# Kernel optimization log

Measured on AMD Instinct MI355X. Metric: run time of the kernel, lower is better.

Reference implementation:

```python
import jax, jax.numpy as jnp
import numpy as np

E = 32  # embedding_dim
B = 1048576

def setup_inputs() -> dict:
    key = jax.random.key(0)
    ks = jax.random.split(key, 16)
    def p(k, shape, scale=0.1):
        return jax.random.normal(k, shape, dtype=jnp.float32) * scale
    return {
        'x': jax.random.normal(ks[0], (B, 2, 5), dtype=jnp.float32),
        'fc_emb_w': p(ks[1], (E, 5)), 'fc_emb_b': p(ks[2], (E,)),
        'in_proj_w': p(ks[3], (3 * E, E)), 'in_proj_b': p(ks[4], (3 * E,)),
        'out_proj_w': p(ks[5], (E, E)), 'out_proj_b': p(ks[6], (E,)),
        'w_ih': p(ks[7], (E, E)), 'b_ih': p(ks[8], (E,)),
        'w_hh': p(ks[9], (E, E)), 'b_hh': p(ks[10], (E,)),
        'fc_dec_w': p(ks[11], (5, E)), 'fc_dec_b': p(ks[12], (5,)),
        'out_w': p(ks[13], (3, 5)), 'out_b': p(ks[14], (3,)),
    }

def gelu(x):
    return jax.nn.gelu(x, approximate=False)  # torch nn.GELU default (erf)

def reference(x, fc_emb_w, fc_emb_b, in_proj_w, in_proj_b,
              out_proj_w, out_proj_b, w_ih, b_ih, w_hh, b_hh,
              fc_dec_w, fc_dec_b, out_w, out_b):
    # per-token embedding: [B,2,5] -> [B,2,E]
    e = gelu(jnp.einsum('bsi,ei->bse', x, fc_emb_w) + fc_emb_b)
    # single-head self-attention (seq_len=2)
    wq, wk, wv = jnp.split(in_proj_w, 3, axis=0)
    bq, bk, bv = jnp.split(in_proj_b, 3, axis=0)
    q = jnp.einsum('bsd,ed->bse', e, wq) + bq
    k = jnp.einsum('bsd,ed->bse', e, wk) + bk
    v = jnp.einsum('bsd,ed->bse', e, wv) + bv
    scores = jnp.einsum('bqd,bkd->bqk', q, k) / jnp.sqrt(jnp.float32(E))
    attn = jax.nn.softmax(scores, axis=-1)
    o = jnp.einsum('bqk,bkd->bqd', attn, v)
    o = jnp.einsum('bsd,ed->bse', o, out_proj_w) + out_proj_b
    # 2-step tanh RNN, h0 = 0; final hidden state only
    h1 = jnp.tanh(o[:, 0] @ w_ih.T + b_ih + b_hh)
    h2 = jnp.tanh(o[:, 1] @ w_ih.T + b_ih + h1 @ w_hh.T + b_hh)
    # decode
    d = gelu(h2 @ fc_dec_w.T + fc_dec_b)
    return d @ out_w.T + out_b  # [B,3]
```

## Files before the change

kernel.cpp:

```cpp
#include <hip/hip_runtime.h>
#include <math.h>

#define BT 256

typedef _Float16 half2v __attribute__((ext_vector_type(2)));
typedef __fp16   fp16x2 __attribute__((ext_vector_type(2)));
typedef _Float16 half8  __attribute__((ext_vector_type(8)));
typedef float    f32x16 __attribute__((ext_vector_type(16)));

union U4H8 { unsigned int u[4]; half8 h; };

__device__ __forceinline__ half2v u2h(unsigned int u){
  union { unsigned int u; half2v h; } c; c.u = u; return c.h;
}
__device__ __forceinline__ unsigned int h2u(half2v h){
  union { unsigned int u; half2v h; } c; c.h = h; return c.u;
}
__device__ __forceinline__ half2v pkrtz(float a, float b){
  union { fp16x2 f; half2v h; } c;
  c.f = __builtin_amdgcn_cvt_pkrtz(a, b);
  return c.h;
}
__device__ __forceinline__ float fdot2(half2v a, half2v b, float c){
  return __builtin_amdgcn_fdot2(a, b, c, false);
}
__device__ __forceinline__ float frcp(float x){ return __builtin_amdgcn_rcpf(x); }

__device__ __forceinline__ unsigned int pk_rne(float a, float b){
  half2v h; h.x = (_Float16)a; h.y = (_Float16)b; return h2u(h);
}

__device__ __forceinline__ half2v gelu_pk(half2v x){
  const _Float16 a0 = (_Float16)0.3989423f,  a1 = (_Float16)-0.0663157f,
                 a2 = (_Float16)0.0096298f,  a3 = (_Float16)-0.00095967f,
                 a4 = (_Float16)0.000048f,   hp = (_Float16)0.5f,
                 hn = (_Float16)-0.5f;
  const half2v A0={a0,a0}, A1={a1,a1}, A2={a2,a2}, A3={a3,a3}, A4={a4,a4};
  const half2v HP={hp,hp}, HN={hn,hn};
  half2v t = x*x;
  half2v q = A4*t + A3;
  q = q*t + A2;
  q = q*t + A1;
  q = q*t + A0;
  half2v u = x*q;
#if __has_builtin(__builtin_elementwise_min)
  u = __builtin_elementwise_max(u, HN);
  u = __builtin_elementwise_min(u, HP);
#else
  u.x = u.x > hp ? hp : (u.x < hn ? hn : u.x);
  u.y = u.y > hp ? hp : (u.y < hn ? hn : u.y);
#endif
  return x*(u + HP);
}

__device__ __forceinline__ half2v tanh_pk(half2v x){
  const _Float16 c0=(_Float16)0.999716f,  c1=(_Float16)-0.328107f,
                 c2=(_Float16)0.116352f,  c3=(_Float16)-0.031255f,
                 c4=(_Float16)0.005038f,  c5=(_Float16)-0.000348f,
                 tp=(_Float16)2.0f,       tn=(_Float16)-2.0f;
  const half2v C0={c0,c0},C1={c1,c1},C2={c2,c2},C3={c3,c3},C4={c4,c4},C5={c5,c5};
  const half2v TP={tp,tp}, TN={tn,tn};
#if __has_builtin(__builtin_elementwise_min)
  x = __builtin_elementwise_max(x, TN);
  x = __builtin_elementwise_min(x, TP);
#else
  x.x = x.x > tp ? tp : (x.x < tn ? tn : x.x);
  x.y = x.y > tp ? tp : (x.y < tn ? tn : x.y);
#endif
  half2v t = x*x;
  half2v p = C5*t + C4;
  p = p*t + C3;
  p = p*t + C2;
  p = p*t + C1;
  p = p*t + C0;
  return x*p;
}

__global__ void prep_kernel(const float* __restrict__ inw, const float* __restrict__ inb,
                            const float* __restrict__ opw, const float* __restrict__ opb,
                            const float* __restrict__ wih, const float* __restrict__ bih,
                            const float* __restrict__ bhh, const float* __restrict__ whh,
                            const float* __restrict__ decw, const float* __restrict__ embw,
                            const float* __restrict__ embb,
                            const float* __restrict__ decb, const float* __restrict__ outw,
                            unsigned int* __restrict__ wsu){
  __shared__ float sQ[1024], sK[1024], sV[1024], sOP[1024], sWI[1024];
  __shared__ float sA[1024], sP[1024], sM[1024], sT[32], sWV[32];
  const float ISS = 0.17677669529663689f;
  int t = threadIdx.x;
  sQ[t]  = inw[t];
  sK[t]  = inw[1024 + t];
  sV[t]  = inw[2048 + t];
  sOP[t] = opw[t];
  sWI[t] = wih[t];
  __syncthreads();
  int tx = t & 31, ty = t >> 5;
  float accA = 0.f, accP = 0.f;
  #pragma unroll
  for (int m = 0; m < 32; m++){
    accA += sQ[m*32 + ty] * sK[m*32 + tx];
    accP += sOP[ty*32 + m] * sV[m*32 + tx];
  }
  sA[ty*32 + tx] = accA;
  sP[ty*32 + tx] = accP;
  if (ty == 0){
    float aw = 0.f;
    #pragma unroll
    for (int m = 0; m < 32; m++) aw += inb[m] * sK[m*32 + tx];
    sWV[tx] = aw;
  }
  if (ty == 1){
    float at = opb[tx];
    #pragma unroll
    for (int m = 0; m < 32; m++) at += sOP[tx*32 + m] * inb[64 + m];
    sT[tx] = at;
  }
  __syncthreads();
  float accM = 0.f;
  #pragma unroll
  for (int m = 0; m < 32; m++) accM += sWI[ty*32 + m] * sP[m*32 + tx];
  sM[ty*32 + tx] = accM;
  if (ty == 2){
    float ab = bih[tx] + bhh[tx];
    #pragma unroll
    for (int m = 0; m < 32; m++) ab += sWI[tx*32 + m] * sT[m];
    ((float*)wsu)[2320 + tx] = ab;
  }
  __syncthreads();
  if (t < 512){
    int r = t >> 4, j = t & 15;
    int c0 = 16*(j>>3) + 8*((j>>1)&1) + 4*((j>>2)&1) + 2*(j&1);
    wsu[t]        = pk_rne(ISS*sA[r*32+c0], ISS*sA[r*32+c0+1]);
    wsu[512 + t]  = pk_rne(sM[r*32+c0],  sM[r*32+c0+1]);
    wsu[1024 + t] = pk_rne(whh[r*32+c0], whh[r*32+c0+1]);
    wsu[1536 + t] = (r < 5) ? pk_rne(decw[r*32+c0], decw[r*32+c0+1]) : 0u;
  } else if (t < 768){
    int q = t - 512, j2 = q >> 3, cc = (q & 7)*2;
    float a = (cc   < 5) ? embw[j2*5+cc]   : 0.f;
    float b = (cc+1 < 5) ? embw[j2*5+cc+1] : ((cc+1 == 5) ? embb[j2] : 0.f);
    wsu[2048 + q] = pk_rne(a, b);
  } else if (t < 784){
    int q = t - 768, gg = q >> 3, j = q & 7;
    int r0 = 2*(j&1) + 8*(j>>1) + 4*gg;
    wsu[2304 + q] = pk_rne(ISS*sWV[r0], ISS*sWV[r0+1]);
  } else if (t < 787){
    int i = t - 784, c = 2*i;
    float a = decb[c];
    float b = (c+1 < 5) ? decb[c+1] : 0.f;
    wsu[2352 + i] = pk_rne(a, b);
  } else if (t < 796){
    int q = t - 787;
    int r = (q >= 6) ? 2 : ((q >= 3) ? 1 : 0);
    int p = q - r*3, c = 2*p;
    float a = outw[r*5 + c];
    float b = (c+1 < 5) ? outw[r*5 + c + 1] : 0.f;
    wsu[2355 + q] = pk_rne(a, b);
  }
}

__device__ __forceinline__ half8 ldfrag(const unsigned int* __restrict__ p){
  U4H8 t; t.u[0]=p[0]; t.u[1]=p[1]; t.u[2]=p[2]; t.u[3]=p[3]; return t.h;
}
__device__ __forceinline__ half8 h8of(const unsigned int* q){
  U4H8 t; t.u[0]=q[0]; t.u[1]=q[1]; t.u[2]=q[2]; t.u[3]=q[3]; return t.h;
}

__device__ __forceinline__ f32x16 ldbias(const float* __restrict__ p, int grp){
  const float4* b = (const float4*)(p + 4*grp);
  float4 q0 = b[0], q1 = b[2], q2 = b[4], q3 = b[6];
  f32x16 c;
  c[0]=q0.x; c[1]=q0.y; c[2]=q0.z; c[3]=q0.w;
  c[4]=q1.x; c[5]=q1.y; c[6]=q1.z; c[7]=q1.w;
  c[8]=q2.x; c[9]=q2.y; c[10]=q2.z; c[11]=q2.w;
  c[12]=q3.x; c[13]=q3.y; c[14]=q3.z; c[15]=q3.w;
  return c;
}

__global__ __launch_bounds__(BT, 4) void fused_kernel(
    const float* __restrict__ x,
    const unsigned int* __restrict__ wsu,
    const float* __restrict__ outb,
    float* __restrict__ y, long long B)
{
  int tid  = threadIdx.x;
  int lane = tid & 63;
  int col  = lane & 31;
  bool g   = (lane >> 5) != 0;
  int grp  = g ? 1 : 0;
  long long eBase = ((long long)blockIdx.x*(BT/64) + (tid>>6)) * 64;
  if (eBase >= B) return;

  const unsigned int* pA = wsu;
  const unsigned int* pM = wsu + 512;
  const unsigned int* pW = wsu + 1024;
  const unsigned int* pD = wsu + 1536;
  const unsigned int* pE = wsu + 2048;
  const unsigned int* pwv = wsu + 2304;
  const float* bMf = (const float*)(wsu + 2320);
  const unsigned int* pdb  = wsu + 2352;
  const unsigned int* pout = wsu + 2355;

  half8 embA = ldfrag(pE + col*8  + grp*4);
  half8 A1   = ldfrag(pA + col*16 + grp*4), A2 = ldfrag(pA + col*16 + 8 + grp*4);
  half8 M1   = ldfrag(pM + col*16 + grp*4), M2 = ldfrag(pM + col*16 + 8 + grp*4);
  half8 W1   = ldfrag(pW + col*16 + grp*4), W2 = ldfrag(pW + col*16 + 8 + grp*4);
  half8 D1   = ldfrag(pD + col*16 + grp*4), D2 = ldfrag(pD + col*16 + 8 + grp*4);
  half2v wv[8];
  #pragma unroll
  for (int j = 0; j < 8; j++) wv[j] = u2h(pwv[grp*8 + j]);

  f32x16 cb_bM = ldbias(bMf, grp);
  f32x16 z16;
  #pragma unroll
  for (int i = 0; i < 16; i++) z16[i] = 0.f;

  U4H8 xb0[2], xb1[2];
  #pragma unroll
  for (int tt = 0; tt < 2; tt++){
    long long e = eBase + 32*tt + col;
    if (e >= B) e = B - 1;
    const float2* xp = (const float2*)(x + e*10ll);
    float2 p0 = xp[0], p1 = xp[1], p2 = xp[2], p3 = xp[3], p4 = xp[4];
    xb0[tt].u[0] = g ? 0u : h2u(pkrtz(p0.x, p0.y));
    xb0[tt].u[1] = g ? 0u : h2u(pkrtz(p1.x, p1.y));
    xb0[tt].u[2] = g ? 0u : h2u(pkrtz(p2.x, 1.0f));
    xb0[tt].u[3] = 0u;
    xb1[tt].u[0] = g ? 0u : h2u(pkrtz(p2.y, p3.x));
    xb1[tt].u[1] = g ? 0u : h2u(pkrtz(p3.y, p4.x));
    xb1[tt].u[2] = g ? 0u : h2u(pkrtz(p4.y, 1.0f));
    xb1[tt].u[3] = 0u;
  }

  f32x16 e0D[2], e1D[2];
  #pragma unroll
  for (int tt = 0; tt < 2; tt++){
    e0D[tt] = __builtin_amdgcn_mfma_f32_32x32x16_f16(embA, xb0[tt].h, z16, 0,0,0);
    e1D[tt] = __builtin_amdgcn_mfma_f32_32x32x16_f16(embA, xb1[tt].h, z16, 0,0,0);
  }
  unsigned int epk[2][8], dlpk[2][8];
  #pragma unroll
  for (int tt = 0; tt < 2; tt++){
    #pragma unroll
    for (int i = 0; i < 8; i++){
      half2v e0h = gelu_pk(pkrtz(e0D[tt][2*i], e0D[tt][2*i+1]));
      half2v e1h = gelu_pk(pkrtz(e1D[tt][2*i], e1D[tt][2*i+1]));
      epk[tt][i]  = h2u(e0h);
      dlpk[tt][i] = h2u(e1h - e0h);
    }
  }

  f32x16 gD[2];
  #pragma unroll
  for (int tt = 0; tt < 2; tt++){
    gD[tt] = __builtin_amdgcn_mfma_f32_32x32x16_f16(A1, h8of(dlpk[tt]), z16, 0,0,0);
    gD[tt] = __builtin_amdgcn_mfma_f32_32x32x16_f16(A2, h8of(dlpk[tt]+4), gD[tt], 0,0,0);
  }
  float a01[2], a11[2];
  #pragma unroll
  for (int tt = 0; tt < 2; tt++){
    float t0 = 0.f, t1 = 0.f, dw = 0.f;
    #pragma unroll
    for (int i = 0; i < 8; i++){
      half2v gp = pkrtz(gD[tt][2*i], gD[tt][2*i+1]);
      t0 = fdot2(u2h(epk[tt][i]),  gp, t0);
      t1 = fdot2(u2h(dlpk[tt][i]), gp, t1);
      dw = fdot2(wv[i], u2h(dlpk[tt][i]), dw);
    }
    t0 += __shfl_xor(t0, 32);
    t1 += __shfl_xor(t1, 32);
    dw += __shfl_xor(dw, 32);
    a01[tt] = frcp(1.0f + __expf(-(t0      + dw)));
    a11[tt] = frcp(1.0f + __expf(-(t0 + t1 + dw)));
  }

  unsigned int c0pk[2][8], c1pk[2][8];
  #pragma unroll
  for (int tt = 0; tt < 2; tt++){
    _Float16 q01 = (_Float16)a01[tt], qda = (_Float16)(a11[tt] - a01[tt]);
    half2v s01 = {q01,q01}, sda = {qda,qda};
    #pragma unroll
    for (int j = 0; j < 8; j++){
      half2v c0 = u2h(dlpk[tt][j])*s01 + u2h(epk[tt][j]);
      half2v c1 = u2h(dlpk[tt][j])*sda + c0;
      c0pk[tt][j] = h2u(c0); c1pk[tt][j] = h2u(c1);
    }
  }

  f32x16 h1D[2];
  #pragma unroll
  for (int tt = 0; tt < 2; tt++){
    h1D[tt] = __builtin_amdgcn_mfma_f32_32x32x16_f16(M1, h8of(c0pk[tt]), cb_bM, 0,0,0);
    h1D[tt] = __builtin_amdgcn_mfma_f32_32x32x16_f16(M2, h8of(c0pk[tt]+4), h1D[tt], 0,0,0);
  }
  unsigned int h1pk[2][8];
  #pragma unroll
  for (int tt = 0; tt < 2; tt++)
    #pragma unroll
    for (int i = 0; i < 8; i++)
      h1pk[tt][i] = h2u(tanh_pk(pkrtz(h1D[tt][2*i], h1D[tt][2*i+1])));

  f32x16 h2D[2];
  #pragma unroll
  for (int tt = 0; tt < 2; tt++){
    h2D[tt] = __builtin_amdgcn_mfma_f32_32x32x16_f16(M1, h8of(c1pk[tt]), cb_bM, 0,0,0);
    h2D[tt] = __builtin_amdgcn_mfma_f32_32x32x16_f16(M2, h8of(c1pk[tt]+4), h2D[tt], 0,0,0);
    h2D[tt] = __builtin_amdgcn_mfma_f32_32x32x16_f16(W1, h8of(h1pk[tt]),   h2D[tt], 0,0,0);
    h2D[tt] = __builtin_amdgcn_mfma_f32_32x32x16_f16(W2, h8of(h1pk[tt]+4), h2D[tt], 0,0,0);
  }
  unsigned int h2pk[2][8];
  #pragma unroll
  for (int tt = 0; tt < 2; tt++)
    #pragma unroll
    for (int i = 0; i < 8; i++)
      h2pk[tt][i] = h2u(tanh_pk(pkrtz(h2D[tt][2*i], h2D[tt][2*i+1])));

  f32x16 dvD[2];
  #pragma unroll
  for (int tt = 0; tt < 2; tt++){
    dvD[tt] = __builtin_amdgcn_mfma_f32_32x32x16_f16(D1, h8of(h2pk[tt]), z16, 0,0,0);
    dvD[tt] = __builtin_amdgcn_mfma_f32_32x32x16_f16(D2, h8of(h2pk[tt]+4), dvD[tt], 0,0,0);
  }
  #pragma unroll
  for (int tt = 0; tt < 2; tt++){
    float dv4 = __shfl_xor(dvD[tt][0], 32);
    half2v dp0 = pkrtz(dvD[tt][0], dvD[tt][1]) + u2h(pdb[0]);
    half2v dp1 = pkrtz(dvD[tt][2], dvD[tt][3]) + u2h(pdb[1]);
    half2v dp2 = pkrtz(dv4,        0.f       ) + u2h(pdb[2]);
    dp0 = gelu_pk(dp0); dp1 = gelu_pk(dp1); dp2 = gelu_pk(dp2);
    float y0 = fdot2(u2h(pout[0]), dp0, fdot2(u2h(pout[1]), dp1, fdot2(u2h(pout[2]), dp2, outb[0])));
    float y1 = fdot2(u2h(pout[3]), dp0, fdot2(u2h(pout[4]), dp1, fdot2(u2h(pout[5]), dp2, outb[1])));
    float y2 = fdot2(u2h(pout[6]), dp0, fdot2(u2h(pout[7]), dp1, fdot2(u2h(pout[8]), dp2, outb[2])));
    long long e = eBase + 32*tt + col;
    if (lane < 32 && e < B){
      float* yp = y + e*3ll;
      yp[0] = y0; yp[1] = y1; yp[2] = y2;
    }
  }
}

extern "C" void kernel_launch(void* const* d_in, const int* in_sizes, int n_in,
                              void* d_out, int out_size, void* d_ws, size_t ws_size,
                              hipStream_t stream){
  const float* x    = (const float*)d_in[0];
  const float* embw = (const float*)d_in[1];
  const float* embb = (const float*)d_in[2];
  const float* inw  = (const float*)d_in[3];
  const float* inb  = (const float*)d_in[4];
  const float* opw  = (const float*)d_in[5];
  const float* opb  = (const float*)d_in[6];
  const float* wih  = (const float*)d_in[7];
  const float* bih  = (const float*)d_in[8];
  const float* whh  = (const float*)d_in[9];
  const float* bhh  = (const float*)d_in[10];
  const float* decw = (const float*)d_in[11];
  const float* decb = (const float*)d_in[12];
  const float* outw = (const float*)d_in[13];
  const float* outb = (const float*)d_in[14];
  float* y = (float*)d_out;
  unsigned int* wsu = (unsigned int*)d_ws;

  long long B = in_sizes[0] / 10;
  long long elems_per_block = (BT/64) * 64;

  prep_kernel<<<1, 1024, 0, stream>>>(inw, inb, opw, opb, wih, bih, bhh,
                                      whh, decw, embw, embb, decb, outw, wsu);
  int grid = (int)((B + elems_per_block - 1)/elems_per_block);
  fused_kernel<<<grid, BT, 0, stream>>>(x, wsu, outb, y, B);
}
```

Baseline: 136.2 us.

## Loop each block over two tiles and swap cross-half shuffles for permlane32_swap

Each block now processes two consecutive 256-element tiles in a loop and the grid is halved. This amortizes the per-wave loading of weight fragments, biases and output bias across more elements. Cross-half reductions use permlane32_swap when the builtin is available instead of ds_bpermute-based shuffles, and the input loads are skipped entirely for the upper half-wave. The price is fewer waves in flight, which could cut latency hiding on the load-bound path.

```diff
diff --git a/kernel.cpp b/kernel.cpp
--- a/kernel.cpp
+++ b/kernel.cpp
@@ -2,6 +2,7 @@
 #include <math.h>
 
 #define BT 256
+#define ITERS 2
 
 typedef _Float16 half2v __attribute__((ext_vector_type(2)));
 typedef __fp16   fp16x2 __attribute__((ext_vector_type(2)));
@@ -28,6 +29,31 @@
 
 __device__ __forceinline__ unsigned int pk_rne(float a, float b){
   half2v h; h.x = (_Float16)a; h.y = (_Float16)b; return h2u(h);
+}
+
+#if __has_builtin(__builtin_amdgcn_permlane32_swap)
+#define HAVE_PLSWAP 1
+#endif
+
+__device__ __forceinline__ float red_sum32(float v){
+#ifdef HAVE_PLSWAP
+  union { float f; unsigned u; } c; c.f = v;
+  auto r = __builtin_amdgcn_permlane32_swap(c.u, c.u, false, false);
+  union { unsigned u; float f; } a, b; a.u = r[0]; b.u = r[1];
+  return a.f + b.f;
+#else
+  return v + __shfl_xor(v, 32);
+#endif
+}
+__device__ __forceinline__ float upper_to_lower(float v){
+#ifdef HAVE_PLSWAP
+  union { float f; unsigned u; } c; c.f = v;
+  auto r = __builtin_amdgcn_permlane32_swap(c.u, c.u, false, false);
+  union { unsigned u; float f; } b; b.u = r[1];
+  return b.f;
+#else
+  return __shfl_xor(v, 32);
+#endif
 }
 
 __device__ __forceinline__ half2v gelu_pk(half2v x){
@@ -187,8 +213,6 @@
   int col  = lane & 31;
   bool g   = (lane >> 5) != 0;
   int grp  = g ? 1 : 0;
-  long long eBase = ((long long)blockIdx.x*(BT/64) + (tid>>6)) * 64;
-  if (eBase >= B) return;
 
   const unsigned int* pA = wsu;
   const unsigned int* pM = wsu + 512;
@@ -210,130 +234,141 @@
   for (int j = 0; j < 8; j++) wv[j] = u2h(pwv[grp*8 + j]);
 
   f32x16 cb_bM = ldbias(bMf, grp);
+  float ob0 = outb[0], ob1 = outb[1], ob2 = outb[2];
   f32x16 z16;
   #pragma unroll
   for (int i = 0; i < 16; i++) z16[i] = 0.f;
 
-  U4H8 xb0[2], xb1[2];
-  #pragma unroll
-  for (int tt = 0; tt < 2; tt++){
-    long long e = eBase + 32*tt + col;
-    if (e >= B) e = B - 1;
-    const float2* xp = (const float2*)(x + e*10ll);
-    float2 p0 = xp[0], p1 = xp[1], p2 = xp[2], p3 = xp[3], p4 = xp[4];
-    xb0[tt].u[0] = g ? 0u : h2u(pkrtz(p0.x, p0.y));
-    xb0[tt].u[1] = g ? 0u : h2u(pkrtz(p1.x, p1.y));
-    xb0[tt].u[2] = g ? 0u : h2u(pkrtz(p2.x, 1.0f));
-    xb0[tt].u[3] = 0u;
-    xb1[tt].u[0] = g ? 0u : h2u(pkrtz(p2.y, p3.x));
-    xb1[tt].u[1] = g ? 0u : h2u(pkrtz(p3.y, p4.x));
-    xb1[tt].u[2] = g ? 0u : h2u(pkrtz(p4.y, 1.0f));
-    xb1[tt].u[3] = 0u;
-  }
-
-  f32x16 e0D[2], e1D[2];
-  #pragma unroll
-  for (int tt = 0; tt < 2; tt++){
-    e0D[tt] = __builtin_amdgcn_mfma_f32_32x32x16_f16(embA, xb0[tt].h, z16, 0,0,0);
-    e1D[tt] = __builtin_amdgcn_mfma_f32_32x32x16_f16(embA, xb1[tt].h, z16, 0,0,0);
-  }
-  unsigned int epk[2][8], dlpk[2][8];
-  #pragma unroll
-  for (int tt = 0; tt < 2; tt++){
-    #pragma unroll
-    for (int i = 0; i < 8; i++){
-      half2v e0h = gelu_pk(pkrtz(e0D[tt][2*i], e0D[tt][2*i+1]));
-      half2v e1h = gelu_pk(pkrtz(e1D[tt][2*i], e1D[tt][2*i+1]));
-      epk[tt][i]  = h2u(e0h);
-      dlpk[tt][i] = h2u(e1h - e0h);
-    }
-  }
-
-  f32x16 gD[2];
-  #pragma unroll
-  for (int tt = 0; tt < 2; tt++){
-    gD[tt] = __builtin_amdgcn_mfma_f32_32x32x16_f16(A1, h8of(dlpk[tt]), z16, 0,0,0);
-    gD[tt] = __builtin_amdgcn_mfma_f32_32x32x16_f16(A2, h8of(dlpk[tt]+4), gD[tt], 0,0,0);
-  }
-  float a01[2], a11[2];
-  #pragma unroll
-  for (int tt = 0; tt < 2; tt++){
-    float t0 = 0.f, t1 = 0.f, dw = 0.f;
-    #pragma unroll
-    for (int i = 0; i < 8; i++){
-      half2v gp = pkrtz(gD[tt][2*i], gD[tt][2*i+1]);
-      t0 = fdot2(u2h(epk[tt][i]),  gp, t0);
-      t1 = fdot2(u2h(dlpk[tt][i]), gp, t1);
-      dw = fdot2(wv[i], u2h(dlpk[tt][i]), dw);
-    }
-    t0 += __shfl_xor(t0, 32);
-    t1 += __shfl_xor(t1, 32);
-    dw += __shfl_xor(dw, 32);
-    a01[tt] = frcp(1.0f + __expf(-(t0      + dw)));
-    a11[tt] = frcp(1.0f + __expf(-(t0 + t1 + dw)));
-  }
-
-  unsigned int c0pk[2][8], c1pk[2][8];
-  #pragma unroll
-  for (int tt = 0; tt < 2; tt++){
-    _Float16 q01 = (_Float16)a01[tt], qda = (_Float16)(a11[tt] - a01[tt]);
-    half2v s01 = {q01,q01}, sda = {qda,qda};
-    #pragma unroll
-    for (int j = 0; j < 8; j++){
-      half2v c0 = u2h(dlpk[tt][j])*s01 + u2h(epk[tt][j]);
-      half2v c1 = u2h(dlpk[tt][j])*sda + c0;
-      c0pk[tt][j] = h2u(c0); c1pk[tt][j] = h2u(c1);
-    }
-  }
-
-  f32x16 h1D[2];
-  #pragma unroll
-  for (int tt = 0; tt < 2; tt++){
-    h1D[tt] = __builtin_amdgcn_mfma_f32_32x32x16_f16(M1, h8of(c0pk[tt]), cb_bM, 0,0,0);
-    h1D[tt] = __builtin_amdgcn_mfma_f32_32x32x16_f16(M2, h8of(c0pk[tt]+4), h1D[tt], 0,0,0);
-  }
-  unsigned int h1pk[2][8];
-  #pragma unroll
-  for (int tt = 0; tt < 2; tt++)
-    #pragma unroll
-    for (int i = 0; i < 8; i++)
-      h1pk[tt][i] = h2u(tanh_pk(pkrtz(h1D[tt][2*i], h1D[tt][2*i+1])));
-
-  f32x16 h2D[2];
-  #pragma unroll
-  for (int tt = 0; tt < 2; tt++){
-    h2D[tt] = __builtin_amdgcn_mfma_f32_32x32x16_f16(M1, h8of(c1pk[tt]), cb_bM, 0,0,0);
-    h2D[tt] = __builtin_amdgcn_mfma_f32_32x32x16_f16(M2, h8of(c1pk[tt]+4), h2D[tt], 0,0,0);
-    h2D[tt] = __builtin_amdgcn_mfma_f32_32x32x16_f16(W1, h8of(h1pk[tt]),   h2D[tt], 0,0,0);
-    h2D[tt] = __builtin_amdgcn_mfma_f32_32x32x16_f16(W2, h8of(h1pk[tt]+4), h2D[tt], 0,0,0);
-  }
-  unsigned int h2pk[2][8];
-  #pragma unroll
-  for (int tt = 0; tt < 2; tt++)
-    #pragma unroll
-    for (int i = 0; i < 8; i++)
-      h2pk[tt][i] = h2u(tanh_pk(pkrtz(h2D[tt][2*i], h2D[tt][2*i+1])));
-
-  f32x16 dvD[2];
-  #pragma unroll
-  for (int tt = 0; tt < 2; tt++){
-    dvD[tt] = __builtin_amdgcn_mfma_f32_32x32x16_f16(D1, h8of(h2pk[tt]), z16, 0,0,0);
-    dvD[tt] = __builtin_amdgcn_mfma_f32_32x32x16_f16(D2, h8of(h2pk[tt]+4), dvD[tt], 0,0,0);
-  }
-  #pragma unroll
-  for (int tt = 0; tt < 2; tt++){
-    float dv4 = __shfl_xor(dvD[tt][0], 32);
-    half2v dp0 = pkrtz(dvD[tt][0], dvD[tt][1]) + u2h(pdb[0]);
-    half2v dp1 = pkrtz(dvD[tt][2], dvD[tt][3]) + u2h(pdb[1]);
-    half2v dp2 = pkrtz(dv4,        0.f       ) + u2h(pdb[2]);
-    dp0 = gelu_pk(dp0); dp1 = gelu_pk(dp1); dp2 = gelu_pk(dp2);
-    float y0 = fdot2(u2h(pout[0]), dp0, fdot2(u2h(pout[1]), dp1, fdot2(u2h(pout[2]), dp2, outb[0])));
-    float y1 = fdot2(u2h(pout[3]), dp0, fdot2(u2h(pout[4]), dp1, fdot2(u2h(pout[5]), dp2, outb[1])));
-    float y2 = fdot2(u2h(pout[6]), dp0, fdot2(u2h(pout[7]), dp1, fdot2(u2h(pout[8]), dp2, outb[2])));
-    long long e = eBase + 32*tt + col;
-    if (lane < 32 && e < B){
-      float* yp = y + e*3ll;
-      yp[0] = y0; yp[1] = y1; yp[2] = y2;
+  for (int it = 0; it < ITERS; ++it){
+    long long eBase = (((long long)blockIdx.x*ITERS + it)*(BT/64) + (tid>>6)) * 64;
+    if (eBase >= B) break;
+
+    U4H8 xb0[2], xb1[2];
+    #pragma unroll
+    for (int tt = 0; tt < 2; tt++){
+      xb0[tt].u[0]=0u; xb0[tt].u[1]=0u; xb0[tt].u[2]=0u; xb0[tt].u[3]=0u;
+      xb1[tt].u[0]=0u; xb1[tt].u[1]=0u; xb1[tt].u[2]=0u; xb1[tt].u[3]=0u;
+    }
+    if (!g){
+      #pragma unroll
+      for (int tt = 0; tt < 2; tt++){
+        long long e = eBase + 32*tt + col;
+        if (e >= B) e = B - 1;
+        const float2* xp = (const float2*)(x + e*10ll);
+        float2 p0 = xp[0], p1 = xp[1], p2 = xp[2], p3 = xp[3], p4 = xp[4];
+        xb0[tt].u[0] = h2u(pkrtz(p0.x, p0.y));
+        xb0[tt].u[1] = h2u(pkrtz(p1.x, p1.y));
+        xb0[tt].u[2] = h2u(pkrtz(p2.x, 1.0f));
+        xb1[tt].u[0] = h2u(pkrtz(p2.y, p3.x));
+        xb1[tt].u[1] = h2u(pkrtz(p3.y, p4.x));
+        xb1[tt].u[2] = h2u(pkrtz(p4.y, 1.0f));
+      }
+    }
+
+    f32x16 e0D[2], e1D[2];
+    #pragma unroll
+    for (int tt = 0; tt < 2; tt++){
+      e0D[tt] = __builtin_amdgcn_mfma_f32_32x32x16_f16(embA, xb0[tt].h, z16, 0,0,0);
+      e1D[tt] = __builtin_amdgcn_mfma_f32_32x32x16_f16(embA, xb1[tt].h, z16, 0,0,0);
+    }
+    unsigned int epk[2][8], dlpk[2][8];
+    #pragma unroll
+    for (int tt = 0; tt < 2; tt++){
+      #pragma unroll
+      for (int i = 0; i < 8; i++){
+        half2v e0h = gelu_pk(pkrtz(e0D[tt][2*i], e0D[tt][2*i+1]));
+        half2v e1h = gelu_pk(pkrtz(e1D[tt][2*i], e1D[tt][2*i+1]));
+        epk[tt][i]  = h2u(e0h);
+        dlpk[tt][i] = h2u(e1h - e0h);
+      }
+    }
+
+    f32x16 gD[2];
+    #pragma unroll
+    for (int tt = 0; tt < 2; tt++){
+      gD[tt] = __builtin_amdgcn_mfma_f32_32x32x16_f16(A1, h8of(dlpk[tt]), z16, 0,0,0);
+      gD[tt] = __builtin_amdgcn_mfma_f32_32x32x16_f16(A2, h8of(dlpk[tt]+4), gD[tt], 0,0,0);
+    }
+    float a01[2], a11[2];
+    #pragma unroll
+    for (int tt = 0; tt < 2; tt++){
+      float t0 = 0.f, t1 = 0.f, dw = 0.f;
+      #pragma unroll
+      for (int i = 0; i < 8; i++){
+        half2v gp = pkrtz(gD[tt][2*i], gD[tt][2*i+1]);
+        t0 = fdot2(u2h(epk[tt][i]),  gp, t0);
+        t1 = fdot2(u2h(dlpk[tt][i]), gp, t1);
+        dw = fdot2(wv[i], u2h(dlpk[tt][i]), dw);
+      }
+      t0 = red_sum32(t0);
+      t1 = red_sum32(t1);
+      dw = red_sum32(dw);
+      a01[tt] = frcp(1.0f + __expf(-(t0      + dw)));
+      a11[tt] = frcp(1.0f + __expf(-(t0 + t1 + dw)));
+    }
+
+    unsigned int c0pk[2][8], c1pk[2][8];
+    #pragma unroll
+    for (int tt = 0; tt < 2; tt++){
+      _Float16 q01 = (_Float16)a01[tt], qda = (_Float16)(a11[tt] - a01[tt]);
+      half2v s01 = {q01,q01}, sda = {qda,qda};
+      #pragma unroll
+      for (int j = 0; j < 8; j++){
+        half2v c0 = u2h(dlpk[tt][j])*s01 + u2h(epk[tt][j]);
+        half2v c1 = u2h(dlpk[tt][j])*sda + c0;
+        c0pk[tt][j] = h2u(c0); c1pk[tt][j] = h2u(c1);
+      }
+    }
+
+    f32x16 h1D[2];
+    #pragma unroll
+    for (int tt = 0; tt < 2; tt++){
+      h1D[tt] = __builtin_amdgcn_mfma_f32_32x32x16_f16(M1, h8of(c0pk[tt]), cb_bM, 0,0,0);
+      h1D[tt] = __builtin_amdgcn_mfma_f32_32x32x16_f16(M2, h8of(c0pk[tt]+4), h1D[tt], 0,0,0);
+    }
+    unsigned int h1pk[2][8];
+    #pragma unroll
+    for (int tt = 0; tt < 2; tt++)
+      #pragma unroll
+      for (int i = 0; i < 8; i++)
+        h1pk[tt][i] = h2u(tanh_pk(pkrtz(h1D[tt][2*i], h1D[tt][2*i+1])));
+
+    f32x16 h2D[2];
+    #pragma unroll
+    for (int tt = 0; tt < 2; tt++){
+      h2D[tt] = __builtin_amdgcn_mfma_f32_32x32x16_f16(M1, h8of(c1pk[tt]), cb_bM, 0,0,0);
+      h2D[tt] = __builtin_amdgcn_mfma_f32_32x32x16_f16(M2, h8of(c1pk[tt]+4), h2D[tt], 0,0,0);
+      h2D[tt] = __builtin_amdgcn_mfma_f32_32x32x16_f16(W1, h8of(h1pk[tt]),   h2D[tt], 0,0,0);
+      h2D[tt] = __builtin_amdgcn_mfma_f32_32x32x16_f16(W2, h8of(h1pk[tt]+4), h2D[tt], 0,0,0);
+    }
+    unsigned int h2pk[2][8];
+    #pragma unroll
+    for (int tt = 0; tt < 2; tt++)
+      #pragma unroll
+      for (int i = 0; i < 8; i++)
+        h2pk[tt][i] = h2u(tanh_pk(pkrtz(h2D[tt][2*i], h2D[tt][2*i+1])));
+
+    f32x16 dvD[2];
+    #pragma unroll
+    for (int tt = 0; tt < 2; tt++){
+      dvD[tt] = __builtin_amdgcn_mfma_f32_32x32x16_f16(D1, h8of(h2pk[tt]), z16, 0,0,0);
+      dvD[tt] = __builtin_amdgcn_mfma_f32_32x32x16_f16(D2, h8of(h2pk[tt]+4), dvD[tt], 0,0,0);
+    }
+    #pragma unroll
+    for (int tt = 0; tt < 2; tt++){
+      float dv4 = upper_to_lower(dvD[tt][0]);
+      half2v dp0 = pkrtz(dvD[tt][0], dvD[tt][1]) + u2h(pdb[0]);
+      half2v dp1 = pkrtz(dvD[tt][2], dvD[tt][3]) + u2h(pdb[1]);
+      half2v dp2 = pkrtz(dv4,        0.f       ) + u2h(pdb[2]);
+      dp0 = gelu_pk(dp0); dp1 = gelu_pk(dp1); dp2 = gelu_pk(dp2);
+      float y0 = fdot2(u2h(pout[0]), dp0, fdot2(u2h(pout[1]), dp1, fdot2(u2h(pout[2]), dp2, ob0)));
+      float y1 = fdot2(u2h(pout[3]), dp0, fdot2(u2h(pout[4]), dp1, fdot2(u2h(pout[5]), dp2, ob1)));
+      float y2 = fdot2(u2h(pout[6]), dp0, fdot2(u2h(pout[7]), dp1, fdot2(u2h(pout[8]), dp2, ob2)));
+      long long e = eBase + 32*tt + col;
+      if (lane < 32 && e < B){
+        float* yp = y + e*3ll;
+        yp[0] = y0; yp[1] = y1; yp[2] = y2;
+      }
     }
   }
 }
@@ -360,7 +395,7 @@
   unsigned int* wsu = (unsigned int*)d_ws;
 
   long long B = in_sizes[0] / 10;
-  long long elems_per_block = (BT/64) * 64;
+  long long elems_per_block = (long long)ITERS * (BT/64) * 64;
 
   prep_kernel<<<1, 1024, 0, stream>>>(inw, inb, opw, opb, wih, bih, bhh,
                                       whh, decw, embw, embb, decb, outw, wsu);
```

New measurement: 143.5 us. +5.3%, slower.
